# Kernel optimization log

Measured on AMD Instinct MI355X. Metric: run time of the kernel, lower is better.

The kernel has to match this reference:

```python
import jax, jax.numpy as jnp
import numpy as np
import math

L, E, H, T, V, B = 8, 1024, 16, 1024, 32000, 2
HD = E // H
EPS = 1e-5


def _quantize_sym(key, shape, std=0.02):
    w = std * jax.random.normal(key, shape, jnp.float32)
    s = jnp.max(jnp.abs(w)) / 127.0  # symmetric int8: 2**(8-1)-1
    q = jnp.clip(jnp.round(w / s), -128, 127).astype(jnp.int8)
    return q, s


def setup_inputs() -> dict:
    key = jax.random.key(0)
    ks = iter(jax.random.split(key, 64 + 16 * L))
    idx = jax.random.randint(next(ks), (B, T), 0, V)
    tok_emb = 0.02 * jax.random.normal(next(ks), (V, E), jnp.float32)
    pos_emb = 0.02 * jax.random.normal(next(ks), (T, E), jnp.float32)
    # per-layer stacked params
    attn_qw, attn_s = [], []
    aproj_qw, aproj_s = [], []
    fc_qw, fc_s = [], []
    mproj_qw, mproj_s = [], []
    for _ in range(L):
        q, s = _quantize_sym(next(ks), (3 * E, E)); attn_qw.append(q); attn_s.append(s)
        q, s = _quantize_sym(next(ks), (E, E)); aproj_qw.append(q); aproj_s.append(s)
        q, s = _quantize_sym(next(ks), (4 * E, E)); fc_qw.append(q); fc_s.append(s)
        q, s = _quantize_sym(next(ks), (E, 4 * E)); mproj_qw.append(q); mproj_s.append(s)
    lm_qw, lm_s = _quantize_sym(next(ks), (V, E))
    return {
        "idx": idx,
        "tok_emb": tok_emb,
        "pos_emb": pos_emb,
        "ln1_g": jnp.ones((L, E)), "ln1_b": jnp.zeros((L, E)),
        "attn_qw": jnp.stack(attn_qw), "attn_s": jnp.stack(attn_s), "attn_b": jnp.zeros((L, 3 * E)),
        "aproj_qw": jnp.stack(aproj_qw), "aproj_s": jnp.stack(aproj_s), "aproj_b": jnp.zeros((L, E)),
        "ln2_g": jnp.ones((L, E)), "ln2_b": jnp.zeros((L, E)),
        "fc_qw": jnp.stack(fc_qw), "fc_s": jnp.stack(fc_s), "fc_b": jnp.zeros((L, 4 * E)),
        "mproj_qw": jnp.stack(mproj_qw), "mproj_s": jnp.stack(mproj_s), "mproj_b": jnp.zeros((L, E)),
        "lnf_g": jnp.ones((E,)), "lnf_b": jnp.zeros((E,)),
        "lm_qw": lm_qw, "lm_s": lm_s,
    }


def _dequant(q, s):
    return q.astype(jnp.float32) * s


def _layernorm(x, g, b):
    m = jnp.mean(x, axis=-1, keepdims=True)
    v = jnp.mean(jnp.square(x - m), axis=-1, keepdims=True)
    return (x - m) * jax.lax.rsqrt(v + EPS) * g + b


def _gpt_forward(idx, tok_emb, pos_emb, ln1_g, ln1_b, attn_qw, attn_s, attn_b,
                 aproj_qw, aproj_s, aproj_b, ln2_g, ln2_b, fc_qw, fc_s, fc_b,
                 mproj_qw, mproj_s, mproj_b, lnf_g, lnf_b, lm_qw, lm_s):
    x = tok_emb[idx] + pos_emb[None, :, :]  # [B,T,E]
    causal = jnp.tril(jnp.ones((T, T), dtype=bool))  # [T,T]
    scale = 1.0 / math.sqrt(HD)

    def block(x, p):
        (l1g, l1b, aqw, asc, ab, pqw, psc, pb,
         l2g, l2b, fqw, fsc, fb, mqw, msc, mb) = p
        h = _layernorm(x, l1g, l1b)
        qkv = h @ _dequant(aqw, asc).T + ab  # [B,T,3E]
        q, k, v = jnp.split(qkv, 3, axis=-1)
        q = q.reshape(B, T, H, HD).transpose(0, 2, 1, 3)  # [B,H,T,HD]
        k = k.reshape(B, T, H, HD).transpose(0, 2, 1, 3)
        v = v.reshape(B, T, H, HD).transpose(0, 2, 1, 3)
        att = jnp.einsum('bhqd,bhkd->bhqk', q, k) * scale
        att = jnp.where(causal, att, -jnp.inf)
        att = jax.nn.softmax(att, axis=-1)
        y = jnp.einsum('bhqk,bhkd->bhqd', att, v)
        y = y.transpose(0, 2, 1, 3).reshape(B, T, E)
        y = y @ _dequant(pqw, psc).T + pb
        x = x + y
        h = _layernorm(x, l2g, l2b)
        h = jax.nn.gelu(h @ _dequant(fqw, fsc).T + fb, approximate=False)
        x = x + h @ _dequant(mqw, msc).T + mb
        return x, None

    layer_params = (ln1_g, ln1_b, attn_qw, attn_s, attn_b,
                    aproj_qw, aproj_s, aproj_b, ln2_g, ln2_b,
                    fc_qw, fc_s, fc_b, mproj_qw, mproj_s, mproj_b)
    x, _ = jax.lax.scan(block, x, layer_params)
    x = _layernorm(x, lnf_g, lnf_b)
    logits = x @ _dequant(lm_qw, lm_s).T  # [B,T,V], no bias
    return logits


def reference(idx, tok_emb, pos_emb, ln1_g, ln1_b, attn_qw, attn_s, attn_b,
              aproj_qw, aproj_s, aproj_b, ln2_g, ln2_b, fc_qw, fc_s, fc_b,
              mproj_qw, mproj_s, mproj_b, lnf_g, lnf_b, lm_qw, lm_s):
    return _gpt_forward(idx, tok_emb, pos_emb, ln1_g, ln1_b, attn_qw, attn_s, attn_b,
                        aproj_qw, aproj_s, aproj_b, ln2_g, ln2_b, fc_qw, fc_s, fc_b,
                        mproj_qw, mproj_s, mproj_b, lnf_g, lnf_b, lm_qw, lm_s)
```

## Files before the change

kernel.cpp:

```cpp
#include <hip/hip_runtime.h>
#include <math.h>

typedef _Float16 h16;
typedef __attribute__((ext_vector_type(8))) _Float16 half8;
typedef __attribute__((ext_vector_type(4))) _Float16 half4;
typedef __attribute__((ext_vector_type(4))) float f32x4;

#define DEVI static __device__ __forceinline__

constexpr int LAY = 8, E = 1024, NH = 16, T = 1024, VOC = 32000, BATCH = 2, HD = 64;
constexpr int MROWS = BATCH * T;
constexpr int E2 = E * E;

DEVI void glds16(const void* g, void* l) {
  __builtin_amdgcn_global_load_lds((const __attribute__((address_space(1))) void*)g,
                                   (__attribute__((address_space(3))) void*)l, 16, 0, 0);
}

__global__ __launch_bounds__(256) void prep_stride_k(const unsigned char* __restrict__ qw1,
                                                     const unsigned char* __restrict__ qw2,
                                                     int* __restrict__ stridew) {
  __shared__ int red2[4], red4[4];
  const int tid = threadIdx.x;
  const int NB = 8192;
  int c2 = 0, c4 = 0;
  for (int i = tid; i < NB; i += 256) {
    const unsigned char b1 = qw1[i], b2 = qw2[i];
    const int s1 = (b1 == 0x00 || b1 == 0xFF) ? 1 : 0;
    const int s2 = (b2 == 0x00 || b2 == 0xFF) ? 1 : 0;
    if (i & 1) c2 += s1 + s2;
    if (i & 3) c4 += s1 + s2;
  }
#pragma unroll
  for (int d = 32; d >= 1; d >>= 1) { c2 += __shfl_xor(c2, d); c4 += __shfl_xor(c4, d); }
  if ((tid & 63) == 0) { red2[tid >> 6] = c2; red4[tid >> 6] = c4; }
  __syncthreads();
  if (tid == 0) {
    const int t2 = red2[0] + red2[1] + red2[2] + red2[3];
    const int t4 = red4[0] + red4[1] + red4[2] + red4[3];
    int stride = 1;
    if (t4 > (NB * 3 / 2) * 98 / 100) stride = 4;
    else if (t2 > NB * 98 / 100) stride = 2;
    stridew[0] = stride;
  }
}

DEVI half8 dq8(const signed char* src, int bstr, float s) {
  half8 o;
  if (bstr == 4) {
    int4 r0 = *reinterpret_cast<const int4*>(src);
    int4 r1 = *reinterpret_cast<const int4*>(src + 16);
    const int* c0 = reinterpret_cast<const int*>(&r0);
    const int* c1 = reinterpret_cast<const int*>(&r1);
#pragma unroll
    for (int j = 0; j < 4; ++j) o[j] = (h16)((float)c0[j] * s);
#pragma unroll
    for (int j = 0; j < 4; ++j) o[4 + j] = (h16)((float)c1[j] * s);
  } else if (bstr == 2) {
    int4 r0 = *reinterpret_cast<const int4*>(src);
    const short* c0 = reinterpret_cast<const short*>(&r0);
#pragma unroll
    for (int j = 0; j < 8; ++j) o[j] = (h16)((float)c0[j] * s);
  } else {
    int2 r0 = *reinterpret_cast<const int2*>(src);
    const signed char* c0 = reinterpret_cast<const signed char*>(&r0);
#pragma unroll
    for (int j = 0; j < 8; ++j) o[j] = (h16)((float)c0[j] * s);
  }
  return o;
}

__global__ __launch_bounds__(256) void dequant_all_k(const signed char* __restrict__ q,
                                                     const int* __restrict__ strideptr,
                                                     const float* __restrict__ sp, int P,
                                                     h16* __restrict__ out, int n) {
  const int i = (blockIdx.x * 256 + threadIdx.x) * 8;
  if (i >= n) return;
  const float s = sp[i / P];
  const int bstr = strideptr[0];
  *reinterpret_cast<half8*>(out + i) = dq8(q + (size_t)i * (size_t)bstr, bstr, s);
}

__global__ __launch_bounds__(256) void dequant_layer_k(
    const signed char* __restrict__ qkv_q, const signed char* __restrict__ ap_q,
    const signed char* __restrict__ fc_q, const signed char* __restrict__ mp_q,
    const float* __restrict__ qkv_s, const float* __restrict__ ap_s,
    const float* __restrict__ fc_s, const float* __restrict__ mp_s, int l,
    const int* __restrict__ strideptr,
    h16* __restrict__ wq, h16* __restrict__ wa, h16* __restrict__ wf,
    h16* __restrict__ wm) {
  const int e = (blockIdx.x * 256 + threadIdx.x) * 8;
  const int bstr = strideptr[0];
  const signed char* src;
  h16* dst;
  float s;
  if (e < 3 * E2) {
    src = qkv_q + ((size_t)l * 3 * E2 + e) * (size_t)bstr;
    dst = wq + e;
    s = qkv_s[l];
  } else if (e < 4 * E2) {
    const int e2 = e - 3 * E2;
    src = ap_q + ((size_t)l * E2 + e2) * (size_t)bstr;
    dst = wa + e2;
    s = ap_s[l];
  } else if (e < 8 * E2) {
    const int e2 = e - 4 * E2;
    src = fc_q + ((size_t)l * 4 * E2 + e2) * (size_t)bstr;
    dst = wf + e2;
    s = fc_s[l];
  } else {
    const int e2 = e - 8 * E2;
    src = mp_q + ((size_t)l * 4 * E2 + e2) * (size_t)bstr;
    dst = wm + e2;
    s = mp_s[l];
  }
  *reinterpret_cast<half8*>(dst) = dq8(src, bstr, s);
}

__global__ __launch_bounds__(256) void embed_k(const int* __restrict__ idx,
                                               const float* __restrict__ tok,
                                               const float* __restrict__ pos,
                                               float* __restrict__ x) {
  const int row = blockIdx.x;
  const int t = row & (T - 1);
  const int id = idx[row];
  const float4 a = reinterpret_cast<const float4*>(tok + (size_t)id * E)[threadIdx.x];
  const float4 p = reinterpret_cast<const float4*>(pos + (size_t)t * E)[threadIdx.x];
  float4 o; o.x = a.x + p.x; o.y = a.y + p.y; o.z = a.z + p.z; o.w = a.w + p.w;
  reinterpret_cast<float4*>(x + (size_t)row * E)[threadIdx.x] = o;
}

__global__ __launch_bounds__(256) void ln_k(const float* __restrict__ x,
                                            const float* __restrict__ g,
                                            const float* __restrict__ bb,
                                            h16* __restrict__ out) {
  __shared__ float red[8];
  const int row = blockIdx.x, tid = threadIdx.x;
  const float4 v = reinterpret_cast<const float4*>(x + (size_t)row * E)[tid];
  float s1 = v.x + v.y + v.z + v.w;
  float s2 = v.x * v.x + v.y * v.y + v.z * v.z + v.w * v.w;
#pragma unroll
  for (int d = 32; d >= 1; d >>= 1) { s1 += __shfl_xor(s1, d); s2 += __shfl_xor(s2, d); }
  if ((tid & 63) == 0) { red[tid >> 6] = s1; red[4 + (tid >> 6)] = s2; }
  __syncthreads();
  s1 = red[0] + red[1] + red[2] + red[3];
  s2 = red[4] + red[5] + red[6] + red[7];
  const float mean = s1 * (1.0f / E);
  const float var = s2 * (1.0f / E) - mean * mean;
  const float rstd = rsqrtf(var + 1e-5f);
  const float4 gv = reinterpret_cast<const float4*>(g)[tid];
  const float4 bv = reinterpret_cast<const float4*>(bb)[tid];
  half4 o;
  o[0] = (h16)((v.x - mean) * rstd * gv.x + bv.x);
  o[1] = (h16)((v.y - mean) * rstd * gv.y + bv.y);
  o[2] = (h16)((v.z - mean) * rstd * gv.z + bv.z);
  o[3] = (h16)((v.w - mean) * rstd * gv.w + bv.w);
  *reinterpret_cast<half4*>(out + (size_t)row * E + tid * 4) = o;
}

__global__ __launch_bounds__(256) void reduce_ln_k(const float* __restrict__ pbuf, int S,
                                                   const float* __restrict__ bias,
                                                   float* __restrict__ x,
                                                   const float* __restrict__ g,
                                                   const float* __restrict__ bb,
                                                   h16* __restrict__ out) {
  __shared__ float red[8];
  const int row = blockIdx.x, tid = threadIdx.x;
  const size_t base = (size_t)row * E + tid * 4;
  float4 a = *reinterpret_cast<const float4*>(pbuf + base);
  for (int s = 1; s < S; ++s) {
    const float4 p = *reinterpret_cast<const float4*>(pbuf + (size_t)s * MROWS * E + base);
    a.x += p.x; a.y += p.y; a.z += p.z; a.w += p.w;
  }
  const float4 bv0 = *reinterpret_cast<const float4*>(bias + tid * 4);
  float4 v = *reinterpret_cast<const float4*>(x + base);
  v.x += a.x + bv0.x; v.y += a.y + bv0.y; v.z += a.z + bv0.z; v.w += a.w + bv0.w;
  *reinterpret_cast<float4*>(x + base) = v;
  float s1 = v.x + v.y + v.z + v.w;
  float s2 = v.x * v.x + v.y * v.y + v.z * v.z + v.w * v.w;
#pragma unroll
  for (int d = 32; d >= 1; d >>= 1) { s1 += __shfl_xor(s1, d); s2 += __shfl_xor(s2, d); }
  if ((tid & 63) == 0) { red[tid >> 6] = s1; red[4 + (tid >> 6)] = s2; }
  __syncthreads();
  s1 = red[0] + red[1] + red[2] + red[3];
  s2 = red[4] + red[5] + red[6] + red[7];
  const float mean = s1 * (1.0f / E);
  const float var = s2 * (1.0f / E) - mean * mean;
  const float rstd = rsqrtf(var + 1e-5f);
  const float4 gv = *reinterpret_cast<const float4*>(g + tid * 4);
  const float4 lb = *reinterpret_cast<const float4*>(bb + tid * 4);
  half4 o;
  o[0] = (h16)((v.x - mean) * rstd * gv.x + lb.x);
  o[1] = (h16)((v.y - mean) * rstd * gv.y + lb.y);
  o[2] = (h16)((v.z - mean) * rstd * gv.z + lb.z);
  o[3] = (h16)((v.w - mean) * rstd * gv.w + lb.w);
  *reinterpret_cast<half4*>(out + (size_t)row * E + tid * 4) = o;
}

template <int OUT_KIND, int DO_GELU, int DO_RESID>
__global__ __launch_bounds__(256) void gemm_bt(const h16* __restrict__ A,
                                               const h16* __restrict__ Bw,
                                               const float* __restrict__ bias,
                                               const float* __restrict__ resid,
                                               void* __restrict__ Cout,
                                               int M, int N, int K, int ldc) {
  __shared__ __align__(16) h16 As[4096];
  __shared__ __align__(16) h16 Bs[4096];
  const int tid = threadIdx.x;
  const int w = tid >> 6, lane = tid & 63;
  const int lin = blockIdx.x;
  const int cpx = gridDim.x >> 3;
  const int swz = (lin & 7) * cpx + (lin >> 3);
  const int m0 = (swz & 15) << 7;
  const int n0 = (swz >> 4) << 7;
  const int wr = w >> 1, wc = w & 1;
  const int lr = lane >> 2, lc8 = (lane & 3) << 3;
  const h16* gA = A + (size_t)(m0 + w * 16 + lr) * K + lc8;
  const h16* gB = Bw + (size_t)(n0 + w * 16 + lr) * K + lc8;
  h16* lA0 = &As[w * 512];
  h16* lB0 = &Bs[w * 512];
  f32x4 acc[4][4] = {};
  const int fl = lane & 15, fk = (lane >> 4) << 3;
  const int nk = K >> 5;
  for (int kt = 0; kt < nk; ++kt) {
    const h16* pa = gA + (kt << 5);
    const h16* pb = gB + (kt << 5);
    glds16(pa, lA0);
    glds16(pa + (size_t)64 * K, lA0 + 2048);
    glds16(pb, lB0);
    glds16(pb + (size_t)64 * K, lB0 + 2048);
    __syncthreads();
    half8 af[4], bfr[4];
#pragma unroll
    for (int mi = 0; mi < 4; ++mi)
      af[mi] = *reinterpret_cast<const half8*>(&As[(wr * 64 + mi * 16 + fl) * 32 + fk]);
#pragma unroll
    for (int ni = 0; ni < 4; ++ni)
      bfr[ni] = *reinterpret_cast<const half8*>(&Bs[(wc * 64 + ni * 16 + fl) * 32 + fk]);
#pragma unroll
    for (int mi = 0; mi < 4; ++mi)
#pragma unroll
      for (int ni = 0; ni < 4; ++ni)
        acc[mi][ni] = __builtin_amdgcn_mfma_f32_16x16x32_f16(af[mi], bfr[ni], acc[mi][ni], 0, 0, 0);
    __syncthreads();
  }
  const int fr4 = (lane >> 4) << 2;
#pragma unroll
  for (int mi = 0; mi < 4; ++mi) {
#pragma unroll
    for (int ni = 0; ni < 4; ++ni) {
      const int col = n0 + wc * 64 + ni * 16 + fl;
      const float bv = bias ? bias[col] : 0.0f;
#pragma unroll
      for (int j = 0; j < 4; ++j) {
        const int row = m0 + wr * 64 + mi * 16 + fr4 + j;
        float v = acc[mi][ni][j] + bv;
        if (DO_GELU) v = 0.5f * v * (1.0f + erff(v * 0.70710678118f));
        if (DO_RESID) v += resid[(size_t)row * ldc + col];
        if (OUT_KIND == 1)
          reinterpret_cast<h16*>(Cout)[(size_t)row * ldc + col] = (h16)v;
        else
          reinterpret_cast<float*>(Cout)[(size_t)row * ldc + col] = v;
      }
    }
  }
}

__global__ __launch_bounds__(512) void gemm_bt256(const h16* __restrict__ A,
                                                  const h16* __restrict__ Bw,
                                                  float* __restrict__ Cout,
                                                  int M, int N, int K) {
  __shared__ __align__(16) h16 As[8192];
  __shared__ __align__(16) h16 Bs[8192];
  const int tid = threadIdx.x;
  const int w = tid >> 6, lane = tid & 63;
  const int lin = blockIdx.x;
  const int cpx = gridDim.x >> 3;
  const int swz = (lin & 7) * cpx + (lin >> 3);
  const int m0 = (swz & 7) << 8;
  const int n0 = (swz >> 3) << 8;
  const int wr = w >> 2, wc = w & 3;
  const int lr = lane >> 2, lc8 = (lane & 3) << 3;
  const h16* gA = A + (size_t)(m0 + w * 16 + lr) * K + lc8;
  const h16* gB = Bw + (size_t)(n0 + w * 16 + lr) * K + lc8;
  h16* lA0 = &As[w * 512];
  h16* lB0 = &Bs[w * 512];
  f32x4 acc[8][4] = {};
  const int fl = lane & 15, fk = (lane >> 4) << 3;
  const int nk = K >> 5;
  for (int kt = 0; kt < nk; ++kt) {
    const h16* pa = gA + (kt << 5);
    const h16* pb = gB + (kt << 5);
    glds16(pa, lA0);
    glds16(pa + (size_t)128 * K, lA0 + 4096);
    glds16(pb, lB0);
    glds16(pb + (size_t)128 * K, lB0 + 4096);
    __syncthreads();
    half8 af[8], bfr[4];
#pragma unroll
    for (int mi = 0; mi < 8; ++mi)
      af[mi] = *reinterpret_cast<const half8*>(&As[(wr * 128 + mi * 16 + fl) * 32 + fk]);
#pragma unroll
    for (int ni = 0; ni < 4; ++ni)
      bfr[ni] = *reinterpret_cast<const half8*>(&Bs[(wc * 64 + ni * 16 + fl) * 32 + fk]);
#pragma unroll
    for (int mi = 0; mi < 8; ++mi)
#pragma unroll
      for (int ni = 0; ni < 4; ++ni)
        acc[mi][ni] = __builtin_amdgcn_mfma_f32_16x16x32_f16(af[mi], bfr[ni], acc[mi][ni], 0, 0, 0);
    __syncthreads();
  }
  const int fr4 = (lane >> 4) << 2;
#pragma unroll
  for (int mi = 0; mi < 8; ++mi)
#pragma unroll
    for (int ni = 0; ni < 4; ++ni) {
      const int col = n0 + wc * 64 + ni * 16 + fl;
#pragma unroll
      for (int j = 0; j < 4; ++j) {
        const int row = m0 + wr * 128 + mi * 16 + fr4 + j;
        Cout[(size_t)row * N + col] = acc[mi][ni][j];
      }
    }
}

__global__ __launch_bounds__(256) void gemm_btk(const h16* __restrict__ A,
                                                const h16* __restrict__ Bw,
                                                float* __restrict__ pbuf,
                                                int M, int N, int Kc, int ldk) {
  __shared__ __align__(16) h16 As[4096];
  __shared__ __align__(16) h16 Bs[4096];
  const int tid = threadIdx.x;
  const int w = tid >> 6, lane = tid & 63;
  const int lin = blockIdx.x;
  const int cpx = gridDim.x >> 3;
  const int swz = (lin & 7) * cpx + (lin >> 3);
  const int m0 = (swz & 15) << 7;
  const int n0 = (swz >> 4) << 7;
  const int s = blockIdx.y;
  const int koff = s * Kc;
  const int wr = w >> 1, wc = w & 1;
  const int lr = lane >> 2, lc8 = (lane & 3) << 3;
  const h16* gA = A + (size_t)(m0 + w * 16 + lr) * ldk + koff + lc8;
  const h16* gB = Bw + (size_t)(n0 + w * 16 + lr) * ldk + koff + lc8;
  h16* lA0 = &As[w * 512];
  h16* lB0 = &Bs[w * 512];
  f32x4 acc[4][4] = {};
  const int fl = lane & 15, fk = (lane >> 4) << 3;
  const int nk = Kc >> 5;
  for (int kt = 0; kt < nk; ++kt) {
    const h16* pa = gA + (kt << 5);
    const h16* pb = gB + (kt << 5);
    glds16(pa, lA0);
    glds16(pa + (size_t)64 * ldk, lA0 + 2048);
    glds16(pb, lB0);
    glds16(pb + (size_t)64 * ldk, lB0 + 2048);
    __syncthreads();
    half8 af[4], bfr[4];
#pragma unroll
    for (int mi = 0; mi < 4; ++mi)
      af[mi] = *reinterpret_cast<const half8*>(&As[(wr * 64 + mi * 16 + fl) * 32 + fk]);
#pragma unroll
    for (int ni = 0; ni < 4; ++ni)
      bfr[ni] = *reinterpret_cast<const half8*>(&Bs[(wc * 64 + ni * 16 + fl) * 32 + fk]);
#pragma unroll
    for (int mi = 0; mi < 4; ++mi)
#pragma unroll
      for (int ni = 0; ni < 4; ++ni)
        acc[mi][ni] = __builtin_amdgcn_mfma_f32_16x16x32_f16(af[mi], bfr[ni], acc[mi][ni], 0, 0, 0);
    __syncthreads();
  }
  float* out = pbuf + (size_t)s * M * N;
  const int fr4 = (lane >> 4) << 2;
#pragma unroll
  for (int mi = 0; mi < 4; ++mi)
#pragma unroll
    for (int ni = 0; ni < 4; ++ni) {
      const int col = n0 + wc * 64 + ni * 16 + fl;
#pragma unroll
      for (int j = 0; j < 4; ++j) {
        const int row = m0 + wr * 64 + mi * 16 + fr4 + j;
        out[(size_t)row * N + col] = acc[mi][ni][j];
      }
    }
}

__global__ __launch_bounds__(256) void attn_k(const h16* __restrict__ qkv,
                                              h16* __restrict__ yout) {
  __shared__ __align__(16) h16 Ks[4096];
  __shared__ __align__(16) h16 VTs[4096];
  __shared__ __align__(16) h16 Ps[4096];
  const int qt = blockIdx.x, bh = blockIdx.y;
  const int b = bh >> 4, h = bh & 15;
  const int tid = threadIdx.x, w = tid >> 6, lane = tid & 63;
  const int fl = lane & 15, fkg = lane >> 4, fk = fkg << 3;
  const size_t rowQ0 = (size_t)b * T + qt * 64 + w * 16;
  const h16* qbase = qkv + (rowQ0 + fl) * 3072 + h * 64;
  const half8 qf0 = *reinterpret_cast<const half8*>(qbase + fk);
  const half8 qf1 = *reinterpret_cast<const half8*>(qbase + 32 + fk);
  f32x4 yacc[4] = {};
  float m_run[4], l_run[4];
#pragma unroll
  for (int j = 0; j < 4; ++j) { m_run[j] = -1e30f; l_run[j] = 0.f; }
  const int q_g0 = qt * 64 + w * 16 + (fkg << 2);
  const int krow = lane >> 3, kcol8 = (lane & 7) << 3;
  const int vrow = tid >> 2, vcol8 = (tid & 3) << 3;
  for (int kt = 0; kt <= qt; ++kt) {
    __syncthreads();
    const size_t kbase = (size_t)b * T + kt * 64;
    const h16* gk = qkv + (kbase + w * 8 + krow) * 3072 + E + h * 64 + kcol8;
    glds16(gk, &Ks[w * 512]);
    glds16(gk + (size_t)32 * 3072, &Ks[2048 + w * 512]);
    {
      const h16* gv = qkv + (kbase + vrow) * 3072 + 2 * E + h * 64 + vcol8;
      const half8 v0 = *reinterpret_cast<const half8*>(gv);
      const half8 v1 = *reinterpret_cast<const half8*>(gv + 32);
#pragma unroll
      for (int e = 0; e < 8; ++e) VTs[(vcol8 + e) * 64 + vrow] = v0[e];
#pragma unroll
      for (int e = 0; e < 8; ++e) VTs[(vcol8 + 32 + e) * 64 + vrow] = v1[e];
    }
    __syncthreads();
    f32x4 sacc[4];
#pragma unroll
    for (int ni = 0; ni < 4; ++ni) {
      const half8 kb0 = *reinterpret_cast<const half8*>(&Ks[(ni * 16 + fl) * 64 + fk]);
      const half8 kb1 = *reinterpret_cast<const half8*>(&Ks[(ni * 16 + fl) * 64 + 32 + fk]);
      f32x4 z = {0.f, 0.f, 0.f, 0.f};
      z = __builtin_amdgcn_mfma_f32_16x16x32_f16(qf0, kb0, z, 0, 0, 0);
      z = __builtin_amdgcn_mfma_f32_16x16x32_f16(qf1, kb1, z, 0, 0, 0);
      sacc[ni] = z;
    }
    float tmax[4] = {-1e30f, -1e30f, -1e30f, -1e30f};
#pragma unroll
    for (int ni = 0; ni < 4; ++ni) {
      const int kcol = kt * 64 + ni * 16 + fl;
#pragma unroll
      for (int j = 0; j < 4; ++j) {
        float sv = sacc[ni][j] * 0.125f;
        sv = (kcol > q_g0 + j) ? -1e30f : sv;
        sacc[ni][j] = sv;
        tmax[j] = fmaxf(tmax[j], sv);
      }
    }
#pragma unroll
    for (int d = 1; d < 16; d <<= 1) {
#pragma unroll
      for (int j = 0; j < 4; ++j) tmax[j] = fmaxf(tmax[j], __shfl_xor(tmax[j], d));
    }
    float sc_old[4], psum[4] = {0.f, 0.f, 0.f, 0.f};
#pragma unroll
    for (int j = 0; j < 4; ++j) {
      const float mn = fmaxf(m_run[j], tmax[j]);
      sc_old[j] = __expf(m_run[j] - mn);
      m_run[j] = mn;
    }
#pragma unroll
    for (int ni = 0; ni < 4; ++ni)
#pragma unroll
      for (int j = 0; j < 4; ++j) {
        const float p = __expf(sacc[ni][j] - m_run[j]);
        sacc[ni][j] = p;
        psum[j] += p;
      }
#pragma unroll
    for (int d = 1; d < 16; d <<= 1) {
#pragma unroll
      for (int j = 0; j < 4; ++j) psum[j] += __shfl_xor(psum[j], d);
    }
#pragma unroll
    for (int j = 0; j < 4; ++j) l_run[j] = l_run[j] * sc_old[j] + psum[j];
#pragma unroll
    for (int di = 0; di < 4; ++di)
#pragma unroll
      for (int j = 0; j < 4; ++j) yacc[di][j] *= sc_old[j];
#pragma unroll
    for (int ni = 0; ni < 4; ++ni)
#pragma unroll
      for (int j = 0; j < 4; ++j)
        Ps[w * 1024 + ((fkg << 2) + j) * 64 + ni * 16 + fl] = (h16)sacc[ni][j];
    __syncthreads();
    const half8 pa0 = *reinterpret_cast<const half8*>(&Ps[w * 1024 + fl * 64 + fk]);
    const half8 pa1 = *reinterpret_cast<const half8*>(&Ps[w * 1024 + fl * 64 + 32 + fk]);
#pragma unroll
    for (int di = 0; di < 4; ++di) {
      const half8 vb0 = *reinterpret_cast<const half8*>(&VTs[(di * 16 + fl) * 64 + fk]);
      const half8 vb1 = *reinterpret_cast<const half8*>(&VTs[(di * 16 + fl) * 64 + 32 + fk]);
      yacc[di] = __builtin_amdgcn_mfma_f32_16x16x32_f16(pa0, vb0, yacc[di], 0, 0, 0);
      yacc[di] = __builtin_amdgcn_mfma_f32_16x16x32_f16(pa1, vb1, yacc[di], 0, 0, 0);
    }
  }
  float rl[4];
#pragma unroll
  for (int j = 0; j < 4; ++j) rl[j] = 1.0f / l_run[j];
  const size_t orow0 = rowQ0 + (fkg << 2);
#pragma unroll
  for (int di = 0; di < 4; ++di)
#pragma unroll
    for (int j = 0; j < 4; ++j)
      yout[(orow0 + j) * E + h * 64 + di * 16 + fl] = (h16)(yacc[di][j] * rl[j]);
}

extern "C" void kernel_launch(void* const* d_in, const int* in_sizes, int n_in,
                              void* d_out, int out_size, void* d_ws, size_t ws_size,
                              hipStream_t stream) {
  (void)in_sizes; (void)n_in; (void)out_size; (void)ws_size;
  const int* idx = (const int*)d_in[0];
  const float* tok = (const float*)d_in[1];
  const float* pos = (const float*)d_in[2];
  const float* ln1g = (const float*)d_in[3];
  const float* ln1b = (const float*)d_in[4];
  const signed char* attn_qw = (const signed char*)d_in[5];
  const float* attn_s = (const float*)d_in[6];
  const float* attn_b = (const float*)d_in[7];
  const signed char* aproj_qw = (const signed char*)d_in[8];
  const float* aproj_s = (const float*)d_in[9];
  const float* aproj_b = (const float*)d_in[10];
  const float* ln2g = (const float*)d_in[11];
  const float* ln2b = (const float*)d_in[12];
  const signed char* fc_qw = (const signed char*)d_in[13];
  const float* fc_s = (const float*)d_in[14];
  const float* fc_b = (const float*)d_in[15];
  const signed char* mproj_qw = (const signed char*)d_in[16];
  const float* mproj_s = (const float*)d_in[17];
  const float* mproj_b = (const float*)d_in[18];
  const float* lnfg = (const float*)d_in[19];
  const float* lnfb = (const float*)d_in[20];
  const signed char* lm_qw = (const signed char*)d_in[21];
  const float* lm_s = (const float*)d_in[22];

  char* ws = (char*)d_ws;
  size_t off = 0;
  auto alloc = [&](size_t bytes) {
    char* p = ws + off;
    off += (bytes + 255) & ~(size_t)255;
    return p;
  };
  float* x = (float*)alloc((size_t)MROWS * E * 4);
  h16* hbuf = (h16*)alloc((size_t)MROWS * E * 2);
  h16* big = (h16*)alloc((size_t)MROWS * 4 * E * 2);
  h16* wq = (h16*)alloc((size_t)3 * E2 * 2);
  h16* wa = (h16*)alloc((size_t)E2 * 2);
  h16* wf = (h16*)alloc((size_t)4 * E2 * 2);
  h16* wm = (h16*)alloc((size_t)4 * E2 * 2);
  float* pbuf = (float*)alloc((size_t)4 * MROWS * E * 4);
  h16* wlm = (h16*)alloc((size_t)VOC * E * 2);
  int* stridew = (int*)alloc(256);
  h16* qkvb = big;
  h16* yb = hbuf;
  h16* hfc = big;

  prep_stride_k<<<1, 256, 0, stream>>>((const unsigned char*)attn_qw,
                                       (const unsigned char*)fc_qw, stridew);
  dequant_all_k<<<VOC * E / 2048, 256, 0, stream>>>(lm_qw, stridew, lm_s, VOC * E,
                                                    wlm, VOC * E);
  embed_k<<<MROWS, 256, 0, stream>>>(idx, tok, pos, x);
  ln_k<<<MROWS, 256, 0, stream>>>(x, ln1g, ln1b, hbuf);

  for (int l = 0; l < LAY; ++l) {
    dequant_layer_k<<<12 * E2 / 2048, 256, 0, stream>>>(
        attn_qw, aproj_qw, fc_qw, mproj_qw, attn_s, aproj_s, fc_s, mproj_s, l,
        stridew, wq, wa, wf, wm);
    gemm_bt<1, 0, 0><<<24 * 16, 256, 0, stream>>>(hbuf, wq, attn_b + l * 3 * E, nullptr,
                                                  qkvb, MROWS, 3 * E, E, 3 * E);
    attn_k<<<dim3(16, 32), 256, 0, stream>>>(qkvb, yb);
    gemm_btk<<<dim3(128, 2), 256, 0, stream>>>(yb, wa, pbuf, MROWS, E, 512, E);
    reduce_ln_k<<<MROWS, 256, 0, stream>>>(pbuf, 2, aproj_b + l * E, x,
                                           ln2g + l * E, ln2b + l * E, hbuf);
    gemm_bt<1, 1, 0><<<32 * 16, 256, 0, stream>>>(hbuf, wf, fc_b + l * 4 * E, nullptr,
                                                  hfc, MROWS, 4 * E, E, 4 * E);
    gemm_btk<<<dim3(128, 4), 256, 0, stream>>>(hfc, wm, pbuf, MROWS, E, 1024, 4 * E);
    const float* ng = (l < LAY - 1) ? (ln1g + (l + 1) * E) : lnfg;
    const float* nb = (l < LAY - 1) ? (ln1b + (l + 1) * E) : lnfb;
    reduce_ln_k<<<MROWS, 256, 0, stream>>>(pbuf, 4, mproj_b + l * E, x, ng, nb, hbuf);
  }
  gemm_bt256<<<1000, 512, 0, stream>>>(hbuf, wlm, (float*)d_out, MROWS, VOC, E);
}
```

Measured before the change: 1.917 ms.

## Double-buffer LDS tiles in GEMM kernels to overlap global loads with MFMA

All three GEMM kernels (gemm_bt, gemm_bt256, gemm_btk) now keep two LDS buffers per operand. Each loop iteration issues the global-to-LDS loads for the next K tile before running the MFMAs on the current tile, and one barrier per iteration replaces the previous two. The aim is to hide global memory latency behind matrix compute. In exchange, LDS use per block doubles, which can lower occupancy. The overlap also depends on the barrier waiting for the async LDS loads to finish only after the compute.

```diff
diff --git a/kernel.cpp b/kernel.cpp
--- a/kernel.cpp
+++ b/kernel.cpp
@@ -204,8 +204,8 @@
                                                const float* __restrict__ resid,
                                                void* __restrict__ Cout,
                                                int M, int N, int K, int ldc) {
-  __shared__ __align__(16) h16 As[4096];
-  __shared__ __align__(16) h16 Bs[4096];
+  __shared__ __align__(16) h16 As[2][4096];
+  __shared__ __align__(16) h16 Bs[2][4096];
   const int tid = threadIdx.x;
   const int w = tid >> 6, lane = tid & 63;
   const int lin = blockIdx.x;
@@ -217,32 +217,36 @@
   const int lr = lane >> 2, lc8 = (lane & 3) << 3;
   const h16* gA = A + (size_t)(m0 + w * 16 + lr) * K + lc8;
   const h16* gB = Bw + (size_t)(n0 + w * 16 + lr) * K + lc8;
-  h16* lA0 = &As[w * 512];
-  h16* lB0 = &Bs[w * 512];
   f32x4 acc[4][4] = {};
   const int fl = lane & 15, fk = (lane >> 4) << 3;
   const int nk = K >> 5;
-  for (int kt = 0; kt < nk; ++kt) {
+  auto stage = [&](int buf, int kt) {
     const h16* pa = gA + (kt << 5);
     const h16* pb = gB + (kt << 5);
-    glds16(pa, lA0);
-    glds16(pa + (size_t)64 * K, lA0 + 2048);
-    glds16(pb, lB0);
-    glds16(pb + (size_t)64 * K, lB0 + 2048);
-    __syncthreads();
+    glds16(pa, &As[buf][w * 512]);
+    glds16(pa + (size_t)64 * K, &As[buf][2048 + w * 512]);
+    glds16(pb, &Bs[buf][w * 512]);
+    glds16(pb + (size_t)64 * K, &Bs[buf][2048 + w * 512]);
+  };
+  stage(0, 0);
+  __syncthreads();
+  int cur = 0;
+  for (int kt = 0; kt < nk; ++kt) {
+    if (kt + 1 < nk) stage(cur ^ 1, kt + 1);
     half8 af[4], bfr[4];
 #pragma unroll
     for (int mi = 0; mi < 4; ++mi)
-      af[mi] = *reinterpret_cast<const half8*>(&As[(wr * 64 + mi * 16 + fl) * 32 + fk]);
+      af[mi] = *reinterpret_cast<const half8*>(&As[cur][(wr * 64 + mi * 16 + fl) * 32 + fk]);
 #pragma unroll
     for (int ni = 0; ni < 4; ++ni)
-      bfr[ni] = *reinterpret_cast<const half8*>(&Bs[(wc * 64 + ni * 16 + fl) * 32 + fk]);
+      bfr[ni] = *reinterpret_cast<const half8*>(&Bs[cur][(wc * 64 + ni * 16 + fl) * 32 + fk]);
 #pragma unroll
     for (int mi = 0; mi < 4; ++mi)
 #pragma unroll
       for (int ni = 0; ni < 4; ++ni)
         acc[mi][ni] = __builtin_amdgcn_mfma_f32_16x16x32_f16(af[mi], bfr[ni], acc[mi][ni], 0, 0, 0);
     __syncthreads();
+    cur ^= 1;
   }
   const int fr4 = (lane >> 4) << 2;
 #pragma unroll
@@ -270,8 +274,8 @@
                                                   const h16* __restrict__ Bw,
                                                   float* __restrict__ Cout,
                                                   int M, int N, int K) {
-  __shared__ __align__(16) h16 As[8192];
-  __shared__ __align__(16) h16 Bs[8192];
+  __shared__ __align__(16) h16 As[2][8192];
+  __shared__ __align__(16) h16 Bs[2][8192];
   const int tid = threadIdx.x;
   const int w = tid >> 6, lane = tid & 63;
   const int lin = blockIdx.x;
@@ -283,32 +287,36 @@
   const int lr = lane >> 2, lc8 = (lane & 3) << 3;
   const h16* gA = A + (size_t)(m0 + w * 16 + lr) * K + lc8;
   const h16* gB = Bw + (size_t)(n0 + w * 16 + lr) * K + lc8;
-  h16* lA0 = &As[w * 512];
-  h16* lB0 = &Bs[w * 512];
   f32x4 acc[8][4] = {};
   const int fl = lane & 15, fk = (lane >> 4) << 3;
   const int nk = K >> 5;
-  for (int kt = 0; kt < nk; ++kt) {
+  auto stage = [&](int buf, int kt) {
     const h16* pa = gA + (kt << 5);
     const h16* pb = gB + (kt << 5);
-    glds16(pa, lA0);
-    glds16(pa + (size_t)128 * K, lA0 + 4096);
-    glds16(pb, lB0);
-    glds16(pb + (size_t)128 * K, lB0 + 4096);
-    __syncthreads();
+    glds16(pa, &As[buf][w * 512]);
+    glds16(pa + (size_t)128 * K, &As[buf][4096 + w * 512]);
+    glds16(pb, &Bs[buf][w * 512]);
+    glds16(pb + (size_t)128 * K, &Bs[buf][4096 + w * 512]);
+  };
+  stage(0, 0);
+  __syncthreads();
+  int cur = 0;
+  for (int kt = 0; kt < nk; ++kt) {
+    if (kt + 1 < nk) stage(cur ^ 1, kt + 1);
     half8 af[8], bfr[4];
 #pragma unroll
     for (int mi = 0; mi < 8; ++mi)
-      af[mi] = *reinterpret_cast<const half8*>(&As[(wr * 128 + mi * 16 + fl) * 32 + fk]);
+      af[mi] = *reinterpret_cast<const half8*>(&As[cur][(wr * 128 + mi * 16 + fl) * 32 + fk]);
 #pragma unroll
     for (int ni = 0; ni < 4; ++ni)
-      bfr[ni] = *reinterpret_cast<const half8*>(&Bs[(wc * 64 + ni * 16 + fl) * 32 + fk]);
+      bfr[ni] = *reinterpret_cast<const half8*>(&Bs[cur][(wc * 64 + ni * 16 + fl) * 32 + fk]);
 #pragma unroll
     for (int mi = 0; mi < 8; ++mi)
 #pragma unroll
       for (int ni = 0; ni < 4; ++ni)
         acc[mi][ni] = __builtin_amdgcn_mfma_f32_16x16x32_f16(af[mi], bfr[ni], acc[mi][ni], 0, 0, 0);
     __syncthreads();
+    cur ^= 1;
   }
   const int fr4 = (lane >> 4) << 2;
 #pragma unroll
@@ -328,8 +336,8 @@
                                                 const h16* __restrict__ Bw,
                                                 float* __restrict__ pbuf,
                                                 int M, int N, int Kc, int ldk) {
-  __shared__ __align__(16) h16 As[4096];
-  __shared__ __align__(16) h16 Bs[4096];
+  __shared__ __align__(16) h16 As[2][4096];
+  __shared__ __align__(16) h16 Bs[2][4096];
   const int tid = threadIdx.x;
   const int w = tid >> 6, lane = tid & 63;
   const int lin = blockIdx.x;
@@ -343,32 +351,36 @@
   const int lr = lane >> 2, lc8 = (lane & 3) << 3;
   const h16* gA = A + (size_t)(m0 + w * 16 + lr) * ldk + koff + lc8;
   const h16* gB = Bw + (size_t)(n0 + w * 16 + lr) * ldk + koff + lc8;
-  h16* lA0 = &As[w * 512];
-  h16* lB0 = &Bs[w * 512];
   f32x4 acc[4][4] = {};
   const int fl = lane & 15, fk = (lane >> 4) << 3;
   const int nk = Kc >> 5;
-  for (int kt = 0; kt < nk; ++kt) {
+  auto stage = [&](int buf, int kt) {
     const h16* pa = gA + (kt << 5);
     const h16* pb = gB + (kt << 5);
-    glds16(pa, lA0);
-    glds16(pa + (size_t)64 * ldk, lA0 + 2048);
-    glds16(pb, lB0);
-    glds16(pb + (size_t)64 * ldk, lB0 + 2048);
-    __syncthreads();
+    glds16(pa, &As[buf][w * 512]);
+    glds16(pa + (size_t)64 * ldk, &As[buf][2048 + w * 512]);
+    glds16(pb, &Bs[buf][w * 512]);
+    glds16(pb + (size_t)64 * ldk, &Bs[buf][2048 + w * 512]);
+  };
+  stage(0, 0);
+  __syncthreads();
+  int cur = 0;
+  for (int kt = 0; kt < nk; ++kt) {
+    if (kt + 1 < nk) stage(cur ^ 1, kt + 1);
     half8 af[4], bfr[4];
 #pragma unroll
     for (int mi = 0; mi < 4; ++mi)
-      af[mi] = *reinterpret_cast<const half8*>(&As[(wr * 64 + mi * 16 + fl) * 32 + fk]);
+      af[mi] = *reinterpret_cast<const half8*>(&As[cur][(wr * 64 + mi * 16 + fl) * 32 + fk]);
 #pragma unroll
     for (int ni = 0; ni < 4; ++ni)
-      bfr[ni] = *reinterpret_cast<const half8*>(&Bs[(wc * 64 + ni * 16 + fl) * 32 + fk]);
+      bfr[ni] = *reinterpret_cast<const half8*>(&Bs[cur][(wc * 64 + ni * 16 + fl) * 32 + fk]);
 #pragma unroll
     for (int mi = 0; mi < 4; ++mi)
 #pragma unroll
       for (int ni = 0; ni < 4; ++ni)
         acc[mi][ni] = __builtin_amdgcn_mfma_f32_16x16x32_f16(af[mi], bfr[ni], acc[mi][ni], 0, 0, 0);
     __syncthreads();
+    cur ^= 1;
   }
   float* out = pbuf + (size_t)s * M * N;
   const int fr4 = (lane >> 4) << 2;
```

Result: faster. 1.828 ms (-4.7%).
